# Optimization experiments

Hardware: AMD Instinct MI355X
Metric: run time of the kernel (lower is better)

## Reference

```python
import jax, jax.numpy as jnp
import numpy as np

D_MODEL = 1024
HEADS = 16
DH = D_MODEL // HEADS
ROPE_THETA = 10000.0


def _rope_cache(T, dh, base, dtype):
    half = dh // 2
    inv_freq = 1.0 / (base ** (jnp.arange(half, dtype=dtype) / half))
    t = jnp.arange(T, dtype=dtype)
    freqs = jnp.outer(t, inv_freq)  # [T, half]
    return jnp.sin(freqs), jnp.cos(freqs)


def _apply_rope(x, sin, cos):
    # x: [B, h, T, dh]; sin/cos: [T, dh//2] broadcast over B,h
    half = sin.shape[-1]
    x1, x2 = x[..., :half], x[..., half:2 * half]
    return jnp.concatenate([x1 * cos - x2 * sin, x1 * sin + x2 * cos], axis=-1)


def setup_inputs() -> dict:
    key = jax.random.key(0)
    ks = jax.random.split(key, 5)
    B, T, D = 4, 2048, D_MODEL
    scale = 1.0 / np.sqrt(D)
    x_btd = jax.random.normal(ks[0], (B, T, D), dtype=jnp.float32)
    Wqkv = jax.random.normal(ks[1], (D, 3 * D), dtype=jnp.float32) * scale
    bqkv = jnp.zeros((3 * D,), dtype=jnp.float32)
    Wproj = jax.random.normal(ks[2], (D, D), dtype=jnp.float32) * scale
    bproj = jnp.zeros((D,), dtype=jnp.float32)
    return {"x_btd": x_btd, "Wqkv": Wqkv, "bqkv": bqkv, "Wproj": Wproj, "bproj": bproj}


def reference(x_btd, Wqkv, bqkv, Wproj, bproj):
    B, T, D = x_btd.shape
    h, dh = HEADS, DH
    qkv = x_btd @ Wqkv + bqkv                      # [B, T, 3D]
    q, k, v = jnp.split(qkv, 3, axis=-1)

    def to_heads(z):
        return z.reshape(B, T, h, dh).transpose(0, 2, 1, 3)  # [B, h, T, dh]

    qh, kh, vh = to_heads(q), to_heads(k), to_heads(v)
    sin, cos = _rope_cache(T, dh, ROPE_THETA, x_btd.dtype)
    qh = _apply_rope(qh, sin, cos)
    kh = _apply_rope(kh, sin, cos)

    scores = jnp.einsum('bhqd,bhkd->bhqk', qh, kh) / jnp.sqrt(jnp.asarray(dh, x_btd.dtype))
    attn = jax.nn.softmax(scores, axis=-1)
    out = jnp.einsum('bhqk,bhkd->bhqd', attn, vh)  # [B, h, T, dh]
    out = out.transpose(0, 2, 1, 3).reshape(B, T, D)
    return out @ Wproj + bproj
```

## Files before the change

### kernel.cpp

```cpp
#include <hip/hip_runtime.h>
#include <stdint.h>


typedef float  f32x4  __attribute__((ext_vector_type(4)));
typedef float  f32x16 __attribute__((ext_vector_type(16)));
typedef short  s16x8  __attribute__((ext_vector_type(8)));
typedef unsigned int u32x4 __attribute__((ext_vector_type(4)));
typedef unsigned short u16;
typedef unsigned int   u32;

#define LOG2E 1.4426950408889634f

__device__ __forceinline__ u16 f2bf(float f) {
  u32 u = __float_as_uint(f);
  u32 r = (u + 0x7fffu + ((u >> 16) & 1u)) >> 16;
  return (u16)r;
}

__device__ __forceinline__ u32 cvtpk_bf16(float lo, float hi) {
  u32 w;
  asm("v_cvt_pk_bf16_f32 %0, %1, %2" : "=v"(w) : "v"(lo), "v"(hi));
  return w;
}

__device__ __forceinline__ void gload_lds16(const u16* g, u16* l) {
  __builtin_amdgcn_global_load_lds(
      (const __attribute__((address_space(1))) uint32_t*)g,
      (__attribute__((address_space(3))) uint32_t*)l, 16, 0, 0);
}

__device__ __forceinline__ float vmax16(f32x16 v) {
  float a = fmaxf(fmaxf(v[0], v[1]), v[2]);
  float b = fmaxf(fmaxf(v[3], v[4]), v[5]);
  float c = fmaxf(fmaxf(v[6], v[7]), v[8]);
  float d = fmaxf(fmaxf(v[9], v[10]), v[11]);
  float e = fmaxf(fmaxf(v[12], v[13]), v[14]);
  float x = fmaxf(fmaxf(a, b), c);
  float y = fmaxf(fmaxf(d, e), v[15]);
  return fmaxf(x, y);
}

__global__ void rope_table_kernel(float* __restrict__ rsin, float* __restrict__ rcos) {
  int idx = blockIdx.x * 256 + threadIdx.x;
  int t = idx >> 5, i = idx & 31;
  float invf = 1.0f / powf(10000.0f, (float)i * (1.0f / 32.0f));
  float ang = (float)t * invf;
  rsin[idx] = sinf(ang);
  rcos[idx] = cosf(ang);
}

__global__ void cvt_bf16_kernel(const float* __restrict__ in, u16* __restrict__ out) {
  int i = blockIdx.x * 256 + threadIdx.x;
  const float4* p = reinterpret_cast<const float4*>(in) + (size_t)i * 2;
  float4 a = p[0], b = p[1];
  u32 w0 = (u32)f2bf(a.x) | ((u32)f2bf(a.y) << 16);
  u32 w1 = (u32)f2bf(a.z) | ((u32)f2bf(a.w) << 16);
  u32 w2 = (u32)f2bf(b.x) | ((u32)f2bf(b.y) << 16);
  u32 w3 = (u32)f2bf(b.z) | ((u32)f2bf(b.w) << 16);
  reinterpret_cast<uint4*>(out)[i] = make_uint4(w0, w1, w2, w3);
}

__global__ void transpose_cvt_kernel(const float* __restrict__ W, u16* __restrict__ Wt,
                                     int rows , int cols ) {
  __shared__ float tile[32][33];
  int k0 = blockIdx.y * 32, n0 = blockIdx.x * 32;
  int t = threadIdx.x;
  int c = t & 31, r0 = t >> 5;
  #pragma unroll
  for (int i = 0; i < 4; i++) {
    int r = r0 + i * 8;
    tile[r][c] = W[(size_t)(k0 + r) * cols + n0 + c];
  }
  __syncthreads();
  int kk = t & 31, nn0 = t >> 5;
  #pragma unroll
  for (int i = 0; i < 4; i++) {
    int nn = nn0 + i * 8;
    Wt[(size_t)(n0 + nn) * rows + k0 + kk] = f2bf(tile[kk][nn]);
  }
}

template<int MODE>
__global__ __launch_bounds__(256) void gemm_kernel(
    const u16* __restrict__ A, const u16* __restrict__ Bt,
    const float* __restrict__ bias,
    const float* __restrict__ rsin, const float* __restrict__ rcos,
    u16* __restrict__ Qg, u16* __restrict__ Kg, u16* __restrict__ Vtg,
    float* __restrict__ Cout, int K)
{
  __shared__ alignas(16) u16 As[128][64];
  __shared__ alignas(16) u16 Bs[128][64];
  int tid = threadIdx.x;
  int lane = tid & 63, wid = tid >> 6;
  int wr = wid >> 1, wc = wid & 1;
  int l15 = lane & 15, lg = lane >> 4;
  int row0 = blockIdx.x * 128, col0 = blockIdx.y * 128;

  f32x4 acc[4][4] = {};

  int sr = lane >> 3, sc = lane & 7;
  int scol = (sc ^ sr) * 8;
  const u16* asrc = A  + (size_t)(row0 + wid * 32 + sr) * K + scol;
  const u16* bsrc = Bt + (size_t)(col0 + wid * 32 + sr) * K + scol;
  u16* aLds = &As[0][0] + wid * 2048;
  u16* bLds = &Bs[0][0] + wid * 2048;

  for (int k0 = 0; k0 < K; k0 += 64) {
    #pragma unroll
    for (int i = 0; i < 4; i++) {
      gload_lds16(asrc + (size_t)(i * 8) * K + k0, aLds + i * 512);
      gload_lds16(bsrc + (size_t)(i * 8) * K + k0, bLds + i * 512);
    }
    __syncthreads();
    #pragma unroll
    for (int kk = 0; kk < 2; kk++) {
      s16x8 af[4], bf[4];
      #pragma unroll
      for (int m = 0; m < 4; m++) {
        int row = wr * 64 + m * 16 + l15;
        int slot = (kk * 4 + lg) ^ (l15 & 7);
        af[m] = *reinterpret_cast<const s16x8*>(&As[row][slot * 8]);
      }
      #pragma unroll
      for (int n = 0; n < 4; n++) {
        int row = wc * 64 + n * 16 + l15;
        int slot = (kk * 4 + lg) ^ (l15 & 7);
        bf[n] = *reinterpret_cast<const s16x8*>(&Bs[row][slot * 8]);
      }
      #pragma unroll
      for (int m = 0; m < 4; m++)
        #pragma unroll
        for (int n = 0; n < 4; n++)
          acc[m][n] = __builtin_amdgcn_mfma_f32_16x16x32_bf16(af[m], bf[n], acc[m][n], 0, 0, 0);
    }
    __syncthreads();
  }

  if (MODE == 0) {
    int wavecol = col0 + wc * 64;
    int sec = wavecol >> 10;
    int h = (wavecol & 1023) >> 6;
    #pragma unroll
    for (int m = 0; m < 4; m++) {
      int rbase = row0 + wr * 64 + m * 16 + lg * 4;
      if (sec < 2) {
        u16* G = (sec == 0) ? Qg : Kg;
        float qs = (sec == 0) ? 0.125f * LOG2E : 1.0f;
        #pragma unroll
        for (int fc = 0; fc < 2; fc++) {
          int dh = fc * 16 + l15;
          float b1 = bias[wavecol + fc * 16 + l15];
          float b2 = bias[wavecol + fc * 16 + l15 + 32];
          #pragma unroll
          for (int j = 0; j < 4; j++) {
            int grow = rbase + j;
            int bidx = grow >> 11, tt = grow & 2047;
            float sn = rsin[tt * 32 + dh], cs = rcos[tt * 32 + dh];
            float v1 = acc[m][fc][j] + b1;
            float v2 = acc[m][fc + 2][j] + b2;
            float lo = (v1 * cs - v2 * sn) * qs;
            float hi = (v1 * sn + v2 * cs) * qs;
            size_t base = ((size_t)(bidx * 16 + h) * 2048 + tt) * 64;
            G[base + dh]      = f2bf(lo);
            G[base + dh + 32] = f2bf(hi);
          }
        }
      } else {
        #pragma unroll
        for (int fc = 0; fc < 4; fc++) {
          int dh = fc * 16 + l15;
          float bb = bias[wavecol + fc * 16 + l15];
          #pragma unroll
          for (int j = 0; j < 4; j++) {
            int grow = rbase + j;
            int bidx = grow >> 11, tt = grow & 2047;
            Vtg[((size_t)(bidx * 16 + h) * 64 + dh) * 2048 + tt] = f2bf(acc[m][fc][j] + bb);
          }
        }
      }
    }
  } else {
    #pragma unroll
    for (int m = 0; m < 4; m++) {
      int grow = row0 + wr * 64 + m * 16 + lg * 4;
      #pragma unroll
      for (int fc = 0; fc < 4; fc++) {
        int col = col0 + wc * 64 + fc * 16 + l15;
        float bb = bias[col];
        #pragma unroll
        for (int j = 0; j < 4; j++)
          Cout[(size_t)(grow + j) * 1024 + col] = acc[m][fc][j] + bb;
      }
    }
  }
}

__global__ __launch_bounds__(512, 4) void attn_kernel(
    const u16* __restrict__ Qg, const u16* __restrict__ Kg, const u16* __restrict__ Vtg,
    u16* __restrict__ Og)
{
  __shared__ alignas(16) u16 Ks[2][4096];
  __shared__ alignas(16) u16 Vs[2][4096];
  int tid = threadIdx.x;
  int lane = tid & 63, wid = tid >> 6;
  int l31 = lane & 31, hi = lane >> 5;
  int bh = blockIdx.x & 63, qt = blockIdx.x >> 6;
  int q = qt * 256 + wid * 32 + l31;
  size_t bh2048 = (size_t)bh * 2048;

  s16x8 aq[4];
  #pragma unroll
  for (int kc = 0; kc < 4; kc++)
    aq[kc] = *reinterpret_cast<const s16x8*>(Qg + (bh2048 + q) * 64 + kc * 16 + hi * 8);

  f32x16 o0 = {}, o1 = {};
  float m_run = -3.0e38f, l_run = 0.f;

  int sr = lane >> 3, sc = lane & 7;
  int scol = (sc ^ sr) * 8;
  const u16* kg_src = Kg + (bh2048 + wid * 8 + sr) * 64 + scol;
  const u16* vg_src = Vtg + ((size_t)bh * 64 + wid * 8 + sr) * 2048 + scol;
  int sdst = wid * 512;

  int offs[2][4];
  #pragma unroll
  for (int c = 0; c < 2; c++)
    #pragma unroll
    for (int j = 0; j < 4; j++)
      offs[c][j] = (c * 32 + l31) * 64 + (((j * 2 + hi) ^ (l31 & 7)) * 8);

#define STAGE(TT, BUF) do { \
    gload_lds16(kg_src + (size_t)(TT) * 4096, &Ks[BUF][sdst]); \
    gload_lds16(vg_src + (size_t)(TT) * 64,   &Vs[BUF][sdst]); \
  } while (0)

#define COMPUTE(B) do { \
    const u16* kb = &Ks[B][0]; \
    const u16* vb = &Vs[B][0]; \
    f32x16 s0 = {}, s1 = {}; \
    __builtin_amdgcn_s_setprio(1); \
    _Pragma("unroll") \
    for (int j = 0; j < 4; j++) { \
      s16x8 kf0 = *reinterpret_cast<const s16x8*>(kb + offs[0][j]); \
      s16x8 kf1 = *reinterpret_cast<const s16x8*>(kb + offs[1][j]); \
      s0 = __builtin_amdgcn_mfma_f32_32x32x16_bf16(kf0, aq[j], s0, 0, 0, 0); \
      s1 = __builtin_amdgcn_mfma_f32_32x32x16_bf16(kf1, aq[j], s1, 0, 0, 0); \
    } \
    __builtin_amdgcn_s_setprio(0); \
    float pm = fmaxf(vmax16(s0), vmax16(s1)); \
    pm = fmaxf(pm, __shfl_xor(pm, 32)); \
    if (!__all(pm - m_run <= 11.5f)) {           \
      float mnew = fmaxf(m_run, pm); \
      float al = exp2f(m_run - mnew); \
      m_run = mnew; l_run *= al; \
      _Pragma("unroll") \
      for (int i = 0; i < 16; i++) { o0[i] *= al; o1[i] *= al; } \
    } \
    float r0 = 0.f, r1 = 0.f, r2 = 0.f, r3 = 0.f; \
    _Pragma("unroll") \
    for (int i = 0; i < 16; i++) { \
      s0[i] = exp2f(s0[i] - m_run); \
      s1[i] = exp2f(s1[i] - m_run); \
    } \
    _Pragma("unroll") \
    for (int i = 0; i < 4; i++) { \
      r0 += s0[i] + s0[i + 8]; \
      r1 += s0[i + 4] + s0[i + 12]; \
      r2 += s1[i] + s1[i + 8]; \
      r3 += s1[i + 4] + s1[i + 12]; \
    } \
    float rs = (r0 + r1) + (r2 + r3); \
    rs += __shfl_xor(rs, 32); \
    l_run += rs; \
    s16x8 pf[4]; \
    _Pragma("unroll") \
    for (int ks = 0; ks < 2; ks++) { \
      int rr = ks * 8; \
      u32 a0 = cvtpk_bf16(s0[rr + 0], s0[rr + 1]); \
      u32 b0 = cvtpk_bf16(s0[rr + 4], s0[rr + 5]); \
      u32 a1 = cvtpk_bf16(s0[rr + 2], s0[rr + 3]); \
      u32 b1 = cvtpk_bf16(s0[rr + 6], s0[rr + 7]); \
      asm volatile("v_permlane32_swap_b32 %0, %1" : "+v"(a0), "+v"(b0)); \
      asm volatile("v_permlane32_swap_b32 %0, %1" : "+v"(a1), "+v"(b1)); \
      u32x4 w = {a0, a1, b0, b1}; \
      pf[ks] = __builtin_bit_cast(s16x8, w); \
    } \
    _Pragma("unroll") \
    for (int ks = 0; ks < 2; ks++) { \
      int rr = ks * 8; \
      u32 a0 = cvtpk_bf16(s1[rr + 0], s1[rr + 1]); \
      u32 b0 = cvtpk_bf16(s1[rr + 4], s1[rr + 5]); \
      u32 a1 = cvtpk_bf16(s1[rr + 2], s1[rr + 3]); \
      u32 b1 = cvtpk_bf16(s1[rr + 6], s1[rr + 7]); \
      asm volatile("v_permlane32_swap_b32 %0, %1" : "+v"(a0), "+v"(b0)); \
      asm volatile("v_permlane32_swap_b32 %0, %1" : "+v"(a1), "+v"(b1)); \
      u32x4 w = {a0, a1, b0, b1}; \
      pf[ks + 2] = __builtin_bit_cast(s16x8, w); \
    } \
    __builtin_amdgcn_s_setprio(1); \
    _Pragma("unroll") \
    for (int ks = 0; ks < 4; ks++) { \
      s16x8 vf = *reinterpret_cast<const s16x8*>(vb + offs[0][ks]); \
      o0 = __builtin_amdgcn_mfma_f32_32x32x16_bf16(vf, pf[ks], o0, 0, 0, 0); \
    } \
    _Pragma("unroll") \
    for (int ks = 0; ks < 4; ks++) { \
      s16x8 vf = *reinterpret_cast<const s16x8*>(vb + offs[1][ks]); \
      o1 = __builtin_amdgcn_mfma_f32_32x32x16_bf16(vf, pf[ks], o1, 0, 0, 0); \
    } \
    __builtin_amdgcn_s_setprio(0); \
  } while (0)

  STAGE(0, 0);
  __syncthreads();

  for (int it = 0; it < 16; it++) {
    STAGE(2 * it + 1, 1);
    COMPUTE(0);
    __syncthreads();
    if (it < 15) STAGE(2 * it + 2, 0);
    COMPUTE(1);
    __syncthreads();
  }
#undef STAGE
#undef COMPUTE

  float inv = 1.0f / l_run;
  int b = bh >> 4, h = bh & 15;
  size_t rowbase = ((size_t)b * 2048 + q) * 1024 + h * 64;
  #pragma unroll
  for (int c2 = 0; c2 < 2; c2++) {
    #pragma unroll
    for (int g = 0; g < 4; g++) {
      float e0 = (c2 ? o1[g * 4 + 0] : o0[g * 4 + 0]) * inv;
      float e1 = (c2 ? o1[g * 4 + 1] : o0[g * 4 + 1]) * inv;
      float e2 = (c2 ? o1[g * 4 + 2] : o0[g * 4 + 2]) * inv;
      float e3 = (c2 ? o1[g * 4 + 3] : o0[g * 4 + 3]) * inv;
      u32 w0 = (u32)f2bf(e0) | ((u32)f2bf(e1) << 16);
      u32 w1 = (u32)f2bf(e2) | ((u32)f2bf(e3) << 16);
      int d = c2 * 32 + g * 8 + hi * 4;
      uint2 val; val.x = w0; val.y = w1;
      *reinterpret_cast<uint2*>(Og + rowbase + d) = val;
    }
  }
}

extern "C" void kernel_launch(void* const* d_in, const int* in_sizes, int n_in,
                              void* d_out, int out_size, void* d_ws, size_t ws_size,
                              hipStream_t stream) {
  const float* x     = (const float*)d_in[0];
  const float* Wqkv  = (const float*)d_in[1];
  const float* bqkv  = (const float*)d_in[2];
  const float* Wproj = (const float*)d_in[3];
  const float* bproj = (const float*)d_in[4];
  float* out = (float*)d_out;

  char* ws = (char*)d_ws;
  size_t off = 0;
  auto alloc = [&](size_t bytes) {
    void* p = ws + off;
    off += (bytes + 255) & ~(size_t)255;
    return p;
  };
  float* rsin  = (float*)alloc((size_t)2048 * 32 * 4);
  float* rcos  = (float*)alloc((size_t)2048 * 32 * 4);
  u16* xb      = (u16*)alloc((size_t)8192 * 1024 * 2);
  u16* Wqkvt   = (u16*)alloc((size_t)3072 * 1024 * 2);
  u16* Wprojt  = (u16*)alloc((size_t)1024 * 1024 * 2);
  u16* Qg      = (u16*)alloc((size_t)64 * 2048 * 64 * 2);
  u16* Kg      = (u16*)alloc((size_t)64 * 2048 * 64 * 2);
  u16* Vtg     = (u16*)alloc((size_t)64 * 2048 * 64 * 2);
  u16* AOg     = (u16*)alloc((size_t)8192 * 1024 * 2);

  rope_table_kernel<<<256, 256, 0, stream>>>(rsin, rcos);
  cvt_bf16_kernel<<<4096, 256, 0, stream>>>(x, xb);
  transpose_cvt_kernel<<<dim3(96, 32), 256, 0, stream>>>(Wqkv, Wqkvt, 1024, 3072);
  transpose_cvt_kernel<<<dim3(32, 32), 256, 0, stream>>>(Wproj, Wprojt, 1024, 1024);
  gemm_kernel<0><<<dim3(64, 24), 256, 0, stream>>>(xb, Wqkvt, bqkv, rsin, rcos,
                                                   Qg, Kg, Vtg, nullptr, 1024);
  attn_kernel<<<512, 512, 0, stream>>>(Qg, Kg, Vtg, AOg);
  gemm_kernel<1><<<dim3(64, 8), 256, 0, stream>>>(AOg, Wprojt, bproj, nullptr, nullptr,
                                                  nullptr, nullptr, nullptr, out, 1024);
}
```

Baseline: 223.5 us.

## Shrink attention blocks, swizzle GEMM tiles, use raw exp2 and packed bf16 stores

```diff
diff --git a/kernel.cpp b/kernel.cpp
--- a/kernel.cpp
+++ b/kernel.cpp
@@ -21,6 +21,12 @@
   u32 w;
   asm("v_cvt_pk_bf16_f32 %0, %1, %2" : "=v"(w) : "v"(lo), "v"(hi));
   return w;
+}
+
+__device__ __forceinline__ float fexp2(float x) {
+  float r;
+  asm("v_exp_f32 %0, %1" : "=v"(r) : "v"(x));
+  return r;
 }
 
 __device__ __forceinline__ void gload_lds16(const u16* g, u16* l) {
@@ -94,7 +100,11 @@
   int lane = tid & 63, wid = tid >> 6;
   int wr = wid >> 1, wc = wid & 1;
   int l15 = lane & 15, lg = lane >> 4;
-  int row0 = blockIdx.x * 128, col0 = blockIdx.y * 128;
+
+  int nwg  = (int)(gridDim.x * gridDim.y);
+  int orig = (int)(blockIdx.y * gridDim.x + blockIdx.x);
+  int swz  = (orig & 7) * (nwg >> 3) + (orig >> 3);
+  int row0 = (swz & 63) * 128, col0 = (swz >> 6) * 128;
 
   f32x4 acc[4][4] = {};
 
@@ -195,7 +205,7 @@
   }
 }
 
-__global__ __launch_bounds__(512, 4) void attn_kernel(
+__global__ __launch_bounds__(256, 3) void attn_kernel(
     const u16* __restrict__ Qg, const u16* __restrict__ Kg, const u16* __restrict__ Vtg,
     u16* __restrict__ Og)
 {
@@ -205,7 +215,7 @@
   int lane = tid & 63, wid = tid >> 6;
   int l31 = lane & 31, hi = lane >> 5;
   int bh = blockIdx.x & 63, qt = blockIdx.x >> 6;
-  int q = qt * 256 + wid * 32 + l31;
+  int q = qt * 128 + wid * 32 + l31;
   size_t bh2048 = (size_t)bh * 2048;
 
   s16x8 aq[4];
@@ -218,9 +228,11 @@
 
   int sr = lane >> 3, sc = lane & 7;
   int scol = (sc ^ sr) * 8;
-  const u16* kg_src = Kg + (bh2048 + wid * 8 + sr) * 64 + scol;
-  const u16* vg_src = Vtg + ((size_t)bh * 64 + wid * 8 + sr) * 2048 + scol;
-  int sdst = wid * 512;
+  const u16* kg0 = Kg  + (bh2048 + wid * 16 + sr) * 64 + scol;
+  const u16* kg1 = kg0 + 8 * 64;
+  const u16* vg0 = Vtg + ((size_t)bh * 64 + wid * 16 + sr) * 2048 + scol;
+  const u16* vg1 = vg0 + 8 * 2048;
+  int sdst = wid * 1024;
 
   int offs[2][4];
   #pragma unroll
@@ -230,8 +242,10 @@
       offs[c][j] = (c * 32 + l31) * 64 + (((j * 2 + hi) ^ (l31 & 7)) * 8);
 
 #define STAGE(TT, BUF) do { \
-    gload_lds16(kg_src + (size_t)(TT) * 4096, &Ks[BUF][sdst]); \
-    gload_lds16(vg_src + (size_t)(TT) * 64,   &Vs[BUF][sdst]); \
+    gload_lds16(kg0 + (size_t)(TT) * 4096, &Ks[BUF][sdst]); \
+    gload_lds16(kg1 + (size_t)(TT) * 4096, &Ks[BUF][sdst + 512]); \
+    gload_lds16(vg0 + (size_t)(TT) * 64,   &Vs[BUF][sdst]); \
+    gload_lds16(vg1 + (size_t)(TT) * 64,   &Vs[BUF][sdst + 512]); \
   } while (0)
 
 #define COMPUTE(B) do { \
@@ -251,17 +265,17 @@
     pm = fmaxf(pm, __shfl_xor(pm, 32)); \
     if (!__all(pm - m_run <= 11.5f)) {           \
       float mnew = fmaxf(m_run, pm); \
-      float al = exp2f(m_run - mnew); \
+      float al = fexp2(m_run - mnew); \
       m_run = mnew; l_run *= al; \
       _Pragma("unroll") \
       for (int i = 0; i < 16; i++) { o0[i] *= al; o1[i] *= al; } \
     } \
+    _Pragma("unroll") \
+    for (int i = 0; i < 16; i++) { \
+      s0[i] = fexp2(s0[i] - m_run); \
+      s1[i] = fexp2(s1[i] - m_run); \
+    } \
     float r0 = 0.f, r1 = 0.f, r2 = 0.f, r3 = 0.f; \
-    _Pragma("unroll") \
-    for (int i = 0; i < 16; i++) { \
-      s0[i] = exp2f(s0[i] - m_run); \
-      s1[i] = exp2f(s1[i] - m_run); \
-    } \
     _Pragma("unroll") \
     for (int i = 0; i < 4; i++) { \
       r0 += s0[i] + s0[i + 8]; \
@@ -336,8 +350,8 @@
       float e1 = (c2 ? o1[g * 4 + 1] : o0[g * 4 + 1]) * inv;
       float e2 = (c2 ? o1[g * 4 + 2] : o0[g * 4 + 2]) * inv;
       float e3 = (c2 ? o1[g * 4 + 3] : o0[g * 4 + 3]) * inv;
-      u32 w0 = (u32)f2bf(e0) | ((u32)f2bf(e1) << 16);
-      u32 w1 = (u32)f2bf(e2) | ((u32)f2bf(e3) << 16);
+      u32 w0 = cvtpk_bf16(e0, e1);
+      u32 w1 = cvtpk_bf16(e2, e3);
       int d = c2 * 32 + g * 8 + hi * 4;
       uint2 val; val.x = w0; val.y = w1;
       *reinterpret_cast<uint2*>(Og + rowbase + d) = val;
@@ -378,7 +392,7 @@
   transpose_cvt_kernel<<<dim3(32, 32), 256, 0, stream>>>(Wproj, Wprojt, 1024, 1024);
   gemm_kernel<0><<<dim3(64, 24), 256, 0, stream>>>(xb, Wqkvt, bqkv, rsin, rcos,
                                                    Qg, Kg, Vtg, nullptr, 1024);
-  attn_kernel<<<512, 512, 0, stream>>>(Qg, Kg, Vtg, AOg);
+  attn_kernel<<<1024, 256, 0, stream>>>(Qg, Kg, Vtg, AOg);
   gemm_kernel<1><<<dim3(64, 8), 256, 0, stream>>>(AOg, Wprojt, bproj, nullptr, nullptr,
                                                   nullptr, nullptr, nullptr, out, 1024);
 }
```

After: 220.3 us. No clear change (-1.4%).
